# Performance work log

Measured on AMD Instinct MI355X. Metric: run time of the kernel, lower is better.

## Reference

```python
import jax, jax.numpy as jnp
import numpy as np

B, SQ, SK, H = 8, 2048, 2048, 256
NH, HD = 4, 64  # num_heads, head_dim


def setup_inputs() -> dict:
    key = jax.random.key(0)
    ks = jax.random.split(key, 9)
    scale = 0.02
    inp = {
        'query': jax.random.normal(ks[0], (B, SQ, H), jnp.float32),
        'key':   jax.random.normal(ks[1], (B, SK, H), jnp.float32),
        'value': jax.random.normal(ks[2], (B, SK, H), jnp.float32),
        'mask':  jax.random.bernoulli(ks[3], 0.9, (B, SQ, SK)),
        'Wq': jax.random.normal(ks[4], (H, H), jnp.float32) * scale,
        'bq': jnp.zeros((H,), jnp.float32),
        'Wk': jax.random.normal(ks[5], (H, H), jnp.float32) * scale,
        'bk': jnp.zeros((H,), jnp.float32),
        'Wv': jax.random.normal(ks[6], (H, H), jnp.float32) * scale,
        'bv': jnp.zeros((H,), jnp.float32),
        'Wo': jax.random.normal(ks[7], (H, H), jnp.float32) * scale,
        'bo': jnp.zeros((H,), jnp.float32),
    }
    return inp


def reference(query, key, value, mask, Wq, bq, Wk, bk, Wv, bv, Wo, bo):
    b = query.shape[0]
    scale = jnp.asarray(HD, query.dtype) ** -0.5
    # torch Linear: x @ W.T + b; reshape to [B, NH, S, HD]
    Q = (query @ Wq.T + bq).reshape(b, -1, NH, HD).transpose(0, 2, 1, 3)
    K = (key   @ Wk.T + bk).reshape(b, -1, NH, HD).transpose(0, 2, 1, 3)
    V = (value @ Wv.T + bv).reshape(b, -1, NH, HD).transpose(0, 2, 1, 3)
    scores = jnp.einsum('bhqd,bhkd->bhqk', Q, K) * scale  # [B,NH,SQ,SK]
    # mask-fixing: rows with no valid key get key 0 unmasked
    mask_sum = mask.sum(axis=-1)  # [B,SQ]
    mask_fixed = mask.at[:, :, 0].set(jnp.where(mask_sum == 0, True, mask[:, :, 0]))
    scores = jnp.where(mask_fixed[:, None, :, :], scores, jnp.asarray(-1e9, scores.dtype))
    attn = jax.nn.softmax(scores, axis=-1)
    attn = jnp.where(jnp.isnan(attn), jnp.zeros_like(attn), attn)  # NaN fix
    out = jnp.einsum('bhqk,bhkd->bhqd', attn, V)
    out = out.transpose(0, 2, 1, 3).reshape(b, -1, H)
    out = out @ Wo.T + bo
    return out, attn
```

## Files before the change

### kernel.cpp

```cpp
#include <hip/hip_runtime.h>
#include <math.h>

#define Bn  8
#define SQn 2048
#define SKn 2048
#define Hn  256
#define NHn 4
#define HDn 64
#define SCALE2 0.1803368801111f

typedef __attribute__((ext_vector_type(4))) float f32x4;
typedef __attribute__((ext_vector_type(4))) unsigned int u32x4;
typedef __attribute__((ext_vector_type(8))) short short8;
typedef unsigned short ushort_t;
typedef unsigned long long ull_t;

__device__ __forceinline__ unsigned short f2bf(float f) {
  unsigned u = __builtin_bit_cast(unsigned, f);
  u += 0x7fffu + ((u >> 16) & 1u);
  return (unsigned short)(u >> 16);
}

__device__ __forceinline__ float fexp2(float x) {
  return __builtin_amdgcn_exp2f(x);
}

__device__ __forceinline__ float bf2f(unsigned short v) {
  unsigned u = (unsigned)v << 16;
  return __builtin_bit_cast(float, u);
}

__device__ __forceinline__ short8 load8f(const float* p) {
  float4 v0 = *(const float4*)p;
  float4 v1 = *(const float4*)(p + 4);
  short8 r;
  r[0] = (short)f2bf(v0.x); r[1] = (short)f2bf(v0.y);
  r[2] = (short)f2bf(v0.z); r[3] = (short)f2bf(v0.w);
  r[4] = (short)f2bf(v1.x); r[5] = (short)f2bf(v1.y);
  r[6] = (short)f2bf(v1.z); r[7] = (short)f2bf(v1.w);
  return r;
}

__device__ __forceinline__ f32x4 mfma16(short8 a, short8 b, f32x4 c) {
  return __builtin_amdgcn_mfma_f32_16x16x32_bf16(a, b, c, 0, 0, 0);
}

__global__ __launch_bounds__(256) void prep_kernel(
    const void* __restrict__ maskp,
    const float* __restrict__ Wq, const float* __restrict__ Wk,
    const float* __restrict__ Wv, const float* __restrict__ Wo,
    const float* __restrict__ Xq, const float* __restrict__ Xk,
    const float* __restrict__ Xv,
    ull_t* __restrict__ mout, ushort_t* __restrict__ Wb,
    ushort_t* __restrict__ Xb)
{
  const int bid = blockIdx.x;
  if (bid < 16) {
    const int g = bid * 256 + threadIdx.x;
    #pragma unroll
    for (int it = 0; it < 8; ++it) {
      const int grp = g + it * 4096;
      const int w = grp >> 13;
      const int off = (grp & 8191) * 8;
      const float* src = w == 0 ? Wq : w == 1 ? Wk : w == 2 ? Wv : Wo;
      *(short8*)(Wb + w * 65536 + off) = load8f(src + off);
    }
    return;
  }
  if (bid < 784) {
    const int g0 = (bid - 16) * 2048 + threadIdx.x;
    #pragma unroll
    for (int it = 0; it < 8; ++it) {
      const int grp = g0 + it * 256;
      const int w = grp >> 19;
      const int off = (grp & 524287) * 8;
      const float* src = w == 0 ? Xq : w == 1 ? Xk : Xv;
      *(short8*)(Xb + (size_t)w * 4194304 + off) = load8f(src + off);
    }
    return;
  }
  const int l = threadIdx.x & 63;
  const unsigned probe = ((const unsigned*)maskp)[l];
  const int isbyte = __any(probe > 1u);
  const int gwave = ((bid - 784) * 256 + threadIdx.x) >> 6;
  const int nwaves = (gridDim.x - 784) * 4;
  const long long total4 = (long long)Bn * SQn * (SKn / 256);
  if (isbyte) {
    for (long long w = gwave; w < total4; w += nwaves) {
      const unsigned char* mp = (const unsigned char*)maskp + w * 256;
      bool n0 = mp[l] != 0,        n1 = mp[64 + l] != 0;
      bool n2 = mp[128 + l] != 0,  n3 = mp[192 + l] != 0;
      ull_t b0 = __ballot(n0), b1 = __ballot(n1);
      ull_t b2 = __ballot(n2), b3 = __ballot(n3);
      if (l == 0) {
        mout[w * 4] = b0; mout[w * 4 + 1] = b1;
        mout[w * 4 + 2] = b2; mout[w * 4 + 3] = b3;
      }
    }
  } else {
    for (long long w = gwave; w < total4; w += nwaves) {
      const int* mp = (const int*)maskp + w * 256;
      bool n0 = mp[l] != 0,        n1 = mp[64 + l] != 0;
      bool n2 = mp[128 + l] != 0,  n3 = mp[192 + l] != 0;
      ull_t b0 = __ballot(n0), b1 = __ballot(n1);
      ull_t b2 = __ballot(n2), b3 = __ballot(n3);
      if (l == 0) {
        mout[w * 4] = b0; mout[w * 4 + 1] = b1;
        mout[w * 4 + 2] = b2; mout[w * 4 + 3] = b3;
      }
    }
  }
}

__global__ __launch_bounds__(256) void proj3_kernel(
    const ushort_t* __restrict__ Xb, const ushort_t* __restrict__ Wb,
    const float* __restrict__ bqp, const float* __restrict__ bkp,
    const float* __restrict__ bvp,
    ushort_t* __restrict__ Qb, ushort_t* __restrict__ Kb,
    ushort_t* __restrict__ Vt)
{
  const int which = blockIdx.z;
  const ushort_t* X = Xb + (size_t)which * 4194304;
  const ushort_t* W = Wb + which * 65536;
  const float* bias = which == 0 ? bqp : which == 1 ? bkp : bvp;
  ushort_t* Y = which == 0 ? Qb : which == 1 ? Kb : Vt;
  const int vtrans = (which == 2);

  const int m0 = blockIdx.x * 64;
  const int n0 = blockIdx.y * 64;
  const int wv = threadIdx.x >> 6;
  const int l  = threadIdx.x & 63;
  const int lr = l & 15, lg = l >> 4;
  const int mrow = m0 + wv * 16 + lr;

  f32x4 acc[4];
  #pragma unroll
  for (int t = 0; t < 4; ++t) acc[t] = (f32x4){0.f, 0.f, 0.f, 0.f};

  const ushort_t* ap = X + (size_t)mrow * Hn + lg * 8;
  for (int k0 = 0; k0 < Hn; k0 += 32) {
    short8 a = *(const short8*)(ap + k0);
    #pragma unroll
    for (int t = 0; t < 4; ++t) {
      short8 bb = *(const short8*)(W + (size_t)(n0 + t * 16 + lr) * Hn + k0 + lg * 8);
      acc[t] = mfma16(a, bb, acc[t]);
    }
  }

  #pragma unroll
  for (int t = 0; t < 4; ++t) {
    const int n = n0 + t * 16 + lr;
    const float bv = bias[n];
    const int h = n >> 6, d = n & 63;
    if (!vtrans) {
      #pragma unroll
      for (int r = 0; r < 4; ++r) {
        const int m = m0 + wv * 16 + lg * 4 + r;
        const int bb = m >> 11, s = m & 2047;
        size_t idx = (((size_t)bb * NHn + h) * SQn + s) * HDn + d;
        Y[idx] = f2bf(acc[t][r] + bv);
      }
    } else {
      const int m = m0 + wv * 16 + lg * 4;
      const int bb = m >> 11, s = m & 2047;
      ushort4 pk;
      pk.x = f2bf(acc[t][0] + bv); pk.y = f2bf(acc[t][1] + bv);
      pk.z = f2bf(acc[t][2] + bv); pk.w = f2bf(acc[t][3] + bv);
      size_t idx = (((size_t)bb * NHn + h) * HDn + d) * (size_t)SKn + s;
      *(ushort4*)(Y + idx) = pk;
    }
  }
}

__global__ __launch_bounds__(512)
__attribute__((amdgpu_waves_per_eu(4, 4)))
void fused_attn_kernel(
    const ushort_t* __restrict__ Qb, const ushort_t* __restrict__ Kb,
    const ushort_t* __restrict__ Vt, const unsigned* __restrict__ maskbits,
    float* __restrict__ attn_out, ushort_t* __restrict__ Ob)
{
  __shared__ float red[8][16];
  __shared__ float Opart[8][16][66];

  const int bid = blockIdx.x;
  const int rt = (bid & 7) * 512 + (bid >> 3);
  const int wv = threadIdx.x >> 6;
  const int l  = threadIdx.x & 63;
  const int lr = l & 15, lg = l >> 4;
  const int bh = rt >> 7;
  const int q0 = (rt & 127) << 4;
  const int b  = bh >> 2, h = bh & 3;
  const int colbase = wv * 256;

  const ushort_t* Qh = Qb + (size_t)bh * SQn * HDn;
  const ushort_t* Kh = Kb + (size_t)bh * SKn * HDn;
  const ushort_t* Vh = Vt + (size_t)bh * HDn * SKn;

  short8 qa0 = *(const short8*)(Qh + (q0 + lr) * HDn + lg * 8);
  short8 qa1 = *(const short8*)(Qh + (q0 + lr) * HDn + 32 + lg * 8);

  const int krA = (lr >> 2) * 8 + (lr & 3);
  const unsigned* mrow = maskbits + ((size_t)b * SQn + q0 + lr) * (SKn / 32) + wv * 8;
  const int bsh = lg * 8;

  short8 pf8[8];
  float lsum = 0.f;
  f32x4 oacc[4];
  #pragma unroll
  for (int dt = 0; dt < 4; ++dt) oacc[dt] = (f32x4){0.f, 0.f, 0.f, 0.f};

  u32x4 mw = *(const u32x4*)mrow;
  #pragma unroll
  for (int s8 = 0; s8 < 8; ++s8) {
    if (s8 == 4) mw = *(const u32x4*)(mrow + 4);
    const int c = colbase + s8 * 32;
    const ushort_t* kp = Kh + (size_t)(c + krA) * HDn + lg * 8;
    short8 ka0 = *(const short8*)(kp);
    short8 ka1 = *(const short8*)(kp + 32);
    short8 kb0 = *(const short8*)(kp + 4 * HDn);
    short8 kb1 = *(const short8*)(kp + 4 * HDn + 32);
    f32x4 za = (f32x4){0.f, 0.f, 0.f, 0.f}, zb = (f32x4){0.f, 0.f, 0.f, 0.f};
    za = mfma16(ka0, qa0, za); za = mfma16(ka1, qa1, za);
    zb = mfma16(kb0, qa0, zb); zb = mfma16(kb1, qa1, zb);

    const ushort_t* vp = Vh + (size_t)lr * SKn + c + lg * 8;
    short8 vb0 = *(const short8*)(vp);
    short8 vb1 = *(const short8*)(vp + 16 * SKn);
    short8 vb2 = *(const short8*)(vp + 32 * SKn);
    short8 vb3 = *(const short8*)(vp + 48 * SKn);

    const unsigned bits = (mw[s8 & 3] >> bsh) & 0xFFu;
    short8 pf;
    #pragma unroll
    for (int j = 0; j < 4; ++j) {
      float pa = ((bits >> j) & 1) ? fexp2(za[j] * SCALE2) : 0.f;
      float pb = ((bits >> (4 + j)) & 1) ? fexp2(zb[j] * SCALE2) : 0.f;
      lsum += pa + pb;
      pf[j] = (short)f2bf(pa);
      pf[4 + j] = (short)f2bf(pb);
    }
    pf8[s8] = pf;
    oacc[0] = mfma16(pf, vb0, oacc[0]);
    oacc[1] = mfma16(pf, vb1, oacc[1]);
    oacc[2] = mfma16(pf, vb2, oacc[2]);
    oacc[3] = mfma16(pf, vb3, oacc[3]);
  }

  lsum += __shfl_xor(lsum, 16);
  lsum += __shfl_xor(lsum, 32);
  if (l < 16) red[wv][lr] = lsum;
  #pragma unroll
  for (int dt = 0; dt < 4; ++dt)
    #pragma unroll
    for (int r = 0; r < 4; ++r)
      Opart[wv][lg * 4 + r][dt * 16 + lr] = oacc[dt][r];
  __syncthreads();

  float gsum = 0.f;
  #pragma unroll
  for (int ww = 0; ww < 8; ++ww) gsum += red[ww][lr];
  const bool rowempty = (gsum == 0.f);
  const float rinv = rowempty ? 0.f : 1.f / gsum;

  float* arow = attn_out + ((size_t)bh * SQn + q0 + lr) * (size_t)SKn;
  #pragma unroll
  for (int s8 = 0; s8 < 8; ++s8) {
    const int c = colbase + s8 * 32;
    float av[8];
    #pragma unroll
    for (int j = 0; j < 8; ++j)
      av[j] = bf2f((unsigned short)pf8[s8][j]) * rinv;
    if (rowempty && s8 == 0 && wv == 0 && lg == 0) av[0] = 1.f;
    *(f32x4*)(arow + c + lg * 8)     = (f32x4){av[0], av[1], av[2], av[3]};
    *(f32x4*)(arow + c + lg * 8 + 4) = (f32x4){av[4], av[5], av[6], av[7]};
  }

  #pragma unroll
  for (int e = threadIdx.x; e < 1024; e += 512) {
    const int row = e >> 6, d = e & 63;
    float gs = 0.f;
    #pragma unroll
    for (int ww = 0; ww < 8; ++ww) gs += red[ww][row];
    float s = 0.f;
    #pragma unroll
    for (int ww = 0; ww < 8; ++ww) s += Opart[ww][row][d];
    float val;
    if (gs == 0.f) {
      val = bf2f(Vh[(size_t)d * SKn]);
    } else {
      val = s / gs;
    }
    Ob[((size_t)b * SQn + q0 + row) * Hn + h * HDn + d] = f2bf(val);
  }
}

__global__ __launch_bounds__(256) void oproj_kernel(
    const unsigned short* __restrict__ A, const ushort_t* __restrict__ Wob,
    const float* __restrict__ bias, float* __restrict__ out)
{
  const int m0 = blockIdx.x * 64;
  const int n0 = blockIdx.y * 64;
  const int wv = threadIdx.x >> 6;
  const int l  = threadIdx.x & 63;
  const int lr = l & 15, lg = l >> 4;
  const int mrow = m0 + wv * 16 + lr;

  f32x4 acc[4];
  #pragma unroll
  for (int t = 0; t < 4; ++t) acc[t] = (f32x4){0.f, 0.f, 0.f, 0.f};

  for (int k0 = 0; k0 < Hn; k0 += 32) {
    short8 a = *(const short8*)(A + (size_t)mrow * Hn + k0 + lg * 8);
    #pragma unroll
    for (int t = 0; t < 4; ++t) {
      short8 bb = *(const short8*)(Wob + (size_t)(n0 + t * 16 + lr) * Hn + k0 + lg * 8);
      acc[t] = mfma16(a, bb, acc[t]);
    }
  }
  #pragma unroll
  for (int t = 0; t < 4; ++t) {
    const int n = n0 + t * 16 + lr;
    const float bv = bias[n];
    #pragma unroll
    for (int r = 0; r < 4; ++r) {
      const int m = m0 + wv * 16 + lg * 4 + r;
      out[(size_t)m * Hn + n] = acc[t][r] + bv;
    }
  }
}

extern "C" void kernel_launch(void* const* d_in, const int* in_sizes, int n_in,
                              void* d_out, int out_size, void* d_ws, size_t ws_size,
                              hipStream_t stream) {
  const float* query = (const float*)d_in[0];
  const float* key_  = (const float*)d_in[1];
  const float* value = (const float*)d_in[2];
  const void*  mask  = d_in[3];
  const float* Wq = (const float*)d_in[4];
  const float* bq = (const float*)d_in[5];
  const float* Wk = (const float*)d_in[6];
  const float* bk = (const float*)d_in[7];
  const float* Wv = (const float*)d_in[8];
  const float* bv = (const float*)d_in[9];
  const float* Wo = (const float*)d_in[10];
  const float* bo = (const float*)d_in[11];

  float* out  = (float*)d_out;
  float* attn = out + (size_t)Bn * SQn * Hn;

  char* ws = (char*)d_ws;
  unsigned short* Qb = (unsigned short*)ws;
  unsigned short* Kb = Qb + (size_t)Bn * SQn * Hn;
  unsigned short* Vt = Kb + (size_t)Bn * SKn * Hn;
  unsigned short* Ob = Vt + (size_t)Bn * SKn * Hn;
  unsigned* mbits = (unsigned*)(Ob + (size_t)Bn * SQn * Hn);
  ushort_t* Wb = (ushort_t*)(mbits + (size_t)Bn * SQn * (SKn / 32));
  ushort_t* Xb = (ushort_t*)attn;

  prep_kernel<<<1808, 256, 0, stream>>>(mask, Wq, Wk, Wv, Wo,
                                        query, key_, value,
                                        (ull_t*)mbits, Wb, Xb);
  proj3_kernel<<<dim3(256, 4, 3), 256, 0, stream>>>(
      Xb, Wb, bq, bk, bv, Qb, Kb, Vt);
  fused_attn_kernel<<<4096, 512, 0, stream>>>(Qb, Kb, Vt, mbits, attn, Ob);
  oproj_kernel<<<dim3(256, 4), 256, 0, stream>>>(Ob, Wb + 3 * 65536, bo, out);
}
```

Baseline: 458.7 us.

## Process two 16-row query tiles per 1024-thread block in fused attention

Doubles the attention block to 1024 threads so each block covers 32 query rows as two groups of eight column waves, halving the grid. The shared Opart buffer is reused for the two groups in turn, with extra barriers, to keep LDS use flat. The aim is to amortise per-block setup and the final reduction and improve scheduling. It adds two more __syncthreads and a serialised reduction phase, and keeps waves_per_eu(4,4) with the larger block, which may change occupancy and register limits.

After: 482.1 us. 5.1% more time.

```diff
diff --git a/kernel.cpp b/kernel.cpp
--- a/kernel.cpp
+++ b/kernel.cpp
@@ -172,35 +172,38 @@
   }
 }
 
-__global__ __launch_bounds__(512)
+__global__ __launch_bounds__(1024)
 __attribute__((amdgpu_waves_per_eu(4, 4)))
 void fused_attn_kernel(
     const ushort_t* __restrict__ Qb, const ushort_t* __restrict__ Kb,
     const ushort_t* __restrict__ Vt, const unsigned* __restrict__ maskbits,
     float* __restrict__ attn_out, ushort_t* __restrict__ Ob)
 {
-  __shared__ float red[8][16];
+  __shared__ float red[16][16];
   __shared__ float Opart[8][16][66];
 
   const int bid = blockIdx.x;
-  const int rt = (bid & 7) * 512 + (bid >> 3);
+  const int rt = (bid & 7) * 256 + (bid >> 3);
   const int wv = threadIdx.x >> 6;
+  const int g  = wv >> 3;
+  const int cw = wv & 7;
   const int l  = threadIdx.x & 63;
   const int lr = l & 15, lg = l >> 4;
-  const int bh = rt >> 7;
-  const int q0 = (rt & 127) << 4;
+  const int bh = rt >> 6;
+  const int q0 = (rt & 63) << 5;
   const int b  = bh >> 2, h = bh & 3;
-  const int colbase = wv * 256;
+  const int colbase = cw * 256;
+  const int qrow = q0 + g * 16;
 
   const ushort_t* Qh = Qb + (size_t)bh * SQn * HDn;
   const ushort_t* Kh = Kb + (size_t)bh * SKn * HDn;
   const ushort_t* Vh = Vt + (size_t)bh * HDn * SKn;
 
-  short8 qa0 = *(const short8*)(Qh + (q0 + lr) * HDn + lg * 8);
-  short8 qa1 = *(const short8*)(Qh + (q0 + lr) * HDn + 32 + lg * 8);
+  short8 qa0 = *(const short8*)(Qh + (qrow + lr) * HDn + lg * 8);
+  short8 qa1 = *(const short8*)(Qh + (qrow + lr) * HDn + 32 + lg * 8);
 
   const int krA = (lr >> 2) * 8 + (lr & 3);
-  const unsigned* mrow = maskbits + ((size_t)b * SQn + q0 + lr) * (SKn / 32) + wv * 8;
+  const unsigned* mrow = maskbits + ((size_t)b * SQn + qrow + lr) * (SKn / 32) + cw * 8;
   const int bsh = lg * 8;
 
   short8 pf8[8];
@@ -249,20 +252,22 @@
   lsum += __shfl_xor(lsum, 16);
   lsum += __shfl_xor(lsum, 32);
   if (l < 16) red[wv][lr] = lsum;
-  #pragma unroll
-  for (int dt = 0; dt < 4; ++dt)
-    #pragma unroll
-    for (int r = 0; r < 4; ++r)
-      Opart[wv][lg * 4 + r][dt * 16 + lr] = oacc[dt][r];
+  if (g == 0) {
+    #pragma unroll
+    for (int dt = 0; dt < 4; ++dt)
+      #pragma unroll
+      for (int r = 0; r < 4; ++r)
+        Opart[cw][lg * 4 + r][dt * 16 + lr] = oacc[dt][r];
+  }
   __syncthreads();
 
   float gsum = 0.f;
   #pragma unroll
-  for (int ww = 0; ww < 8; ++ww) gsum += red[ww][lr];
+  for (int ww = 0; ww < 8; ++ww) gsum += red[g * 8 + ww][lr];
   const bool rowempty = (gsum == 0.f);
   const float rinv = rowempty ? 0.f : 1.f / gsum;
 
-  float* arow = attn_out + ((size_t)bh * SQn + q0 + lr) * (size_t)SKn;
+  float* arow = attn_out + ((size_t)bh * SQn + qrow + lr) * (size_t)SKn;
   #pragma unroll
   for (int s8 = 0; s8 < 8; ++s8) {
     const int c = colbase + s8 * 32;
@@ -270,27 +275,43 @@
     #pragma unroll
     for (int j = 0; j < 8; ++j)
       av[j] = bf2f((unsigned short)pf8[s8][j]) * rinv;
-    if (rowempty && s8 == 0 && wv == 0 && lg == 0) av[0] = 1.f;
+    if (rowempty && s8 == 0 && cw == 0 && lg == 0) av[0] = 1.f;
     *(f32x4*)(arow + c + lg * 8)     = (f32x4){av[0], av[1], av[2], av[3]};
     *(f32x4*)(arow + c + lg * 8 + 4) = (f32x4){av[4], av[5], av[6], av[7]};
   }
 
-  #pragma unroll
-  for (int e = threadIdx.x; e < 1024; e += 512) {
-    const int row = e >> 6, d = e & 63;
+  {
+    const int row = threadIdx.x >> 6, d = threadIdx.x & 63;
     float gs = 0.f;
     #pragma unroll
     for (int ww = 0; ww < 8; ++ww) gs += red[ww][row];
     float s = 0.f;
     #pragma unroll
     for (int ww = 0; ww < 8; ++ww) s += Opart[ww][row][d];
-    float val;
-    if (gs == 0.f) {
-      val = bf2f(Vh[(size_t)d * SKn]);
-    } else {
-      val = s / gs;
-    }
+    float val = (gs == 0.f) ? bf2f(Vh[(size_t)d * SKn]) : s / gs;
     Ob[((size_t)b * SQn + q0 + row) * Hn + h * HDn + d] = f2bf(val);
+  }
+  __syncthreads();
+
+  if (g == 1) {
+    #pragma unroll
+    for (int dt = 0; dt < 4; ++dt)
+      #pragma unroll
+      for (int r = 0; r < 4; ++r)
+        Opart[cw][lg * 4 + r][dt * 16 + lr] = oacc[dt][r];
+  }
+  __syncthreads();
+
+  {
+    const int row = threadIdx.x >> 6, d = threadIdx.x & 63;
+    float gs = 0.f;
+    #pragma unroll
+    for (int ww = 0; ww < 8; ++ww) gs += red[8 + ww][row];
+    float s = 0.f;
+    #pragma unroll
+    for (int ww = 0; ww < 8; ++ww) s += Opart[ww][row][d];
+    float val = (gs == 0.f) ? bf2f(Vh[(size_t)d * SKn]) : s / gs;
+    Ob[((size_t)b * SQn + q0 + 16 + row) * Hn + h * HDn + d] = f2bf(val);
   }
 }
 
@@ -362,6 +383,6 @@
                                         (ull_t*)mbits, Wb, Xb);
   proj3_kernel<<<dim3(256, 4, 3), 256, 0, stream>>>(
       Xb, Wb, bq, bk, bv, Qb, Kb, Vt);
-  fused_attn_kernel<<<4096, 512, 0, stream>>>(Qb, Kb, Vt, mbits, attn, Ob);
+  fused_attn_kernel<<<2048, 1024, 0, stream>>>(Qb, Kb, Vt, mbits, attn, Ob);
   oproj_kernel<<<dim3(256, 4), 256, 0, stream>>>(Ob, Wb + 3 * 65536, bo, out);
 }
```
